# Optimization experiments

Hardware: AMD Instinct MI355X
Metric: run time of the kernel (lower is better)

## Reference

```python
import jax, jax.numpy as jnp
import numpy as np

E = 256

def setup_inputs() -> dict:
    key = jax.random.key(0)
    ks = jax.random.split(key, 10)
    N, T_y, T_x = 8, 300, 160
    s = 1.0 / np.sqrt(E)  # torch-style uniform-ish init scale, keeps gates unsaturated
    return {
        "inputs": jax.random.normal(ks[0], (N, T_y, E // 2), jnp.float32),
        "memory": jax.random.normal(ks[1], (N, T_x, E), jnp.float32),
        "h0": jnp.zeros((1, N, E), jnp.float32),
        "Wih": jax.random.normal(ks[2], (3 * E, E // 2), jnp.float32) * s,
        "Whh": jax.random.normal(ks[3], (3 * E, E), jnp.float32) * s,
        "bih": jax.random.normal(ks[4], (3 * E,), jnp.float32) * s,
        "bhh": jax.random.normal(ks[5], (3 * E,), jnp.float32) * s,
        "W": jax.random.normal(ks[6], (E, E), jnp.float32) * s,
        "U": jax.random.normal(ks[7], (E, E), jnp.float32) * s,
        "v": jax.random.normal(ks[8], (E,), jnp.float32) * s,
    }


def reference(inputs, memory, h0, Wih, Whh, bih, bhh, W, U, v):
    # GRU (PyTorch gate order r, z, n), batch_first, single layer, unidirectional.
    def step(h, x_t):
        gi = x_t @ Wih.T + bih      # [N, 3E]
        gh = h @ Whh.T + bhh        # [N, 3E]
        ir, iz, i_n = jnp.split(gi, 3, axis=-1)
        hr, hz, hn = jnp.split(gh, 3, axis=-1)
        r = jax.nn.sigmoid(ir + hr)
        z = jax.nn.sigmoid(iz + hz)
        n = jnp.tanh(i_n + r * hn)
        h_new = (1.0 - z) * n + z * h
        return h_new, h_new

    h_last, outs = jax.lax.scan(step, h0[0], jnp.swapaxes(inputs, 0, 1))
    outputs = jnp.swapaxes(outs, 0, 1)   # [N, T_y, E]
    hidden = h_last[None]                # [1, N, E]

    # Bahdanau additive attention
    w = outputs @ W.T                    # [N, T_y, E]
    u = memory @ U.T                     # [N, T_x, E]
    # scores: v . tanh(w + u) broadcast over [N, T_y, T_x, E]
    scores = jnp.einsum('ntxe,e->ntx', jnp.tanh(w[:, :, None, :] + u[:, None, :, :]), v)
    attn_weights = jax.nn.softmax(scores, axis=2)  # [N, T_y, T_x]
    return attn_weights, outputs, hidden
```

## Files before the change

### kernel.cpp

```cpp
#include <hip/hip_runtime.h>


typedef _Float16 f16x2 __attribute__((ext_vector_type(2)));
typedef _Float16 f16x8 __attribute__((ext_vector_type(8)));
typedef float f32x4 __attribute__((ext_vector_type(4)));

__device__ __forceinline__ float fexp2(float x) { return __builtin_amdgcn_exp2f(x); }
__device__ __forceinline__ float frcp(float x) { return __builtin_amdgcn_rcpf(x); }
__device__ __forceinline__ float fsig(float x) {
    return frcp(1.0f + fexp2(x * -1.4426950408889634f));
}
__device__ __forceinline__ float ftanh(float x) {
    return 1.0f - 2.0f * frcp(1.0f + fexp2(x * 2.8853900817779268f));
}

__device__ __forceinline__ float pick4(f32x4 v, int s) {
    float ab = (s & 1) ? v[1] : v[0];
    float cd = (s & 1) ? v[3] : v[2];
    return (s & 2) ? cd : ab;
}

__global__ __launch_bounds__(256) void phase1_kernel(
    const float* __restrict__ Whh, unsigned* __restrict__ wd,
    const float* __restrict__ inputs, const float* __restrict__ Wih,
    float* __restrict__ gi, const float* __restrict__ bih,
    const float* __restrict__ bhh, int* flags, int full) {
    if (full && blockIdx.x == 0 && threadIdx.x < 10) flags[threadIdx.x] = 0;
    if (blockIdx.x < 384) {
        int gid = blockIdx.x * 256 + threadIdx.x;
        int i = gid >> 9, t = gid & 511;
        int fi = i >> 2, j = i & 3;
        int g = fi >> 4, m2 = (fi >> 3) & 1, ks = fi & 7;
        int w = t >> 6, l = t & 63;
        int row = 256 * g + 32 * w + 16 * m2 + (l & 15);
        int k = 32 * ks + 8 * (l >> 4) + 2 * j;
        union { unsigned u; f16x2 h; } cv;
        cv.h[0] = (_Float16)Whh[(size_t)row * 256 + k];
        cv.h[1] = (_Float16)Whh[(size_t)row * 256 + k + 1];
        wd[i * 512 + t] = cv.u;
        return;
    }
    int id = blockIdx.x - 384;
    const int n0 = (id % 12) * 64, m0 = (id / 12) * 64;
    __shared__ float Xs[32][65];
    __shared__ float Ws2[32][65];
    const int tid = threadIdx.x;
    const int tx = tid & 15, ty = tid >> 4;
    const int M = 2400, K = 128;
    float acc[4][4] = {};
    for (int k0 = 0; k0 < K; k0 += 32) {
#pragma unroll
        for (int i = 0; i < 8; ++i) {
            int e = tid + i * 256;
            int kk = e & 31, m = e >> 5;
            int row = m0 + m;
            Xs[kk][m] = (row < M) ? inputs[(size_t)row * K + k0 + kk] : 0.0f;
            Ws2[kk][m] = Wih[(size_t)(n0 + m) * K + k0 + kk];
        }
        __syncthreads();
#pragma unroll
        for (int kk = 0; kk < 32; ++kk) {
            float a[4], b[4];
#pragma unroll
            for (int i = 0; i < 4; ++i) a[i] = Xs[kk][ty * 4 + i];
#pragma unroll
            for (int j = 0; j < 4; ++j) b[j] = Ws2[kk][tx * 4 + j];
#pragma unroll
            for (int i = 0; i < 4; ++i)
#pragma unroll
                for (int j = 0; j < 4; ++j) acc[i][j] += a[i] * b[j];
        }
        __syncthreads();
    }
#pragma unroll
    for (int i = 0; i < 4; ++i) {
        int row = m0 + ty * 4 + i;
        if (row >= M) continue;
        int b = row / 300;
        int t = row - b * 300;
#pragma unroll
        for (int j = 0; j < 4; ++j) {
            int col = n0 + tx * 4 + j;
            float val = acc[i][j] + ((col < 512) ? (bih[col] + bhh[col]) : bih[col]);
            gi[(size_t)(t * 8 + b) * 768 + col] = val;
        }
    }
}

__global__ __launch_bounds__(256) void gemm_kernel(
    const float* __restrict__ X, const float* __restrict__ Wt,
    float* __restrict__ C, _Float16* __restrict__ C16,
    int M, int N, int K, int mode) {
    __shared__ float Xs[32][65];
    __shared__ float Ws2[32][65];
    const int n0 = blockIdx.x * 64, m0 = blockIdx.y * 64;
    const int tid = threadIdx.x;
    const int tx = tid & 15, ty = tid >> 4;
    float acc[4][4] = {};
    for (int k0 = 0; k0 < K; k0 += 32) {
#pragma unroll
        for (int i = 0; i < 8; ++i) {
            int e = tid + i * 256;
            int kk = e & 31, m = e >> 5;
            int row = m0 + m;
            Xs[kk][m] = (row < M) ? X[(size_t)row * K + k0 + kk] : 0.0f;
            Ws2[kk][m] = Wt[(size_t)(n0 + m) * K + k0 + kk];
        }
        __syncthreads();
#pragma unroll
        for (int kk = 0; kk < 32; ++kk) {
            float a[4], b[4];
#pragma unroll
            for (int i = 0; i < 4; ++i) a[i] = Xs[kk][ty * 4 + i];
#pragma unroll
            for (int j = 0; j < 4; ++j) b[j] = Ws2[kk][tx * 4 + j];
#pragma unroll
            for (int i = 0; i < 4; ++i)
#pragma unroll
                for (int j = 0; j < 4; ++j) acc[i][j] += a[i] * b[j];
        }
        __syncthreads();
    }
#pragma unroll
    for (int i = 0; i < 4; ++i) {
        int row = m0 + ty * 4 + i;
        if (row >= M) continue;
#pragma unroll
        for (int j = 0; j < 4; ++j) {
            int col = n0 + tx * 4 + j;
            if (mode == 2) C16[(size_t)row * N + col] = (_Float16)acc[i][j];
            else           C[(size_t)row * N + col] = acc[i][j];
        }
    }
}

__global__ __launch_bounds__(512, 1) void gru_mega(
    const float* __restrict__ gi, const unsigned* __restrict__ wd,
    const float* __restrict__ h0, const float* __restrict__ bhh,
    float* __restrict__ outs, float* __restrict__ hid,
    const float* __restrict__ memory, const float* __restrict__ Um,
    _Float16* __restrict__ u16, const float* __restrict__ W,
    const float* __restrict__ vv, float* __restrict__ attn,
    int* flags, int full) {
    __shared__ __align__(16) _Float16 hbuf[2][256];
    __shared__ float Xs[32][65];
    __shared__ float Ws2[32][65];
    __shared__ unsigned uS[160 * 129];
    __shared__ __align__(16) float oL[10][260];
    __shared__ float wLf[10][256];
    __shared__ float vL[256], sc[160], red[2];

    const int tid = threadIdx.x;

    if (blockIdx.x >= 8) {
        int id = blockIdx.x - 8;
        if (id < 80) {
            const int n0 = (id & 3) * 64, m0 = (id >> 2) * 64;
            const int tx = tid & 15, ty = (tid & 255) >> 4;
            float acc[4][4] = {};
            for (int k0 = 0; k0 < 256; k0 += 32) {
                if (tid < 256) {
#pragma unroll
                    for (int i = 0; i < 8; ++i) {
                        int e = tid + i * 256;
                        int kk = e & 31, m = e >> 5;
                        Xs[kk][m] = memory[(size_t)(m0 + m) * 256 + k0 + kk];
                        Ws2[kk][m] = Um[(size_t)(n0 + m) * 256 + k0 + kk];
                    }
                }
                __syncthreads();
                if (tid < 256) {
#pragma unroll
                    for (int kk = 0; kk < 32; ++kk) {
                        float a[4], b[4];
#pragma unroll
                        for (int i = 0; i < 4; ++i) a[i] = Xs[kk][ty * 4 + i];
#pragma unroll
                        for (int j = 0; j < 4; ++j) b[j] = Ws2[kk][tx * 4 + j];
#pragma unroll
                        for (int i = 0; i < 4; ++i)
#pragma unroll
                            for (int j = 0; j < 4; ++j) acc[i][j] += a[i] * b[j];
                    }
                }
                __syncthreads();
            }
            if (tid < 256) {
#pragma unroll
                for (int i = 0; i < 4; ++i)
#pragma unroll
                    for (int j = 0; j < 4; ++j)
                        u16[(size_t)(m0 + ty * 4 + i) * 256 + n0 + tx * 4 + j] =
                            (_Float16)acc[i][j];
            }
            if (!full) return;
            __syncthreads();
            if (tid == 0)
                __hip_atomic_fetch_add(&flags[8], 1, __ATOMIC_RELEASE,
                                       __HIP_MEMORY_SCOPE_AGENT);
        }
        if (!full) return;

        const int grp = id / 30;
        const int tc = id % 30;
        if (tid == 0) {
            while (__hip_atomic_load(&flags[8], __ATOMIC_RELAXED,
                                     __HIP_MEMORY_SCOPE_AGENT) < 80)
                __builtin_amdgcn_s_sleep(32);
            while (__hip_atomic_load(&flags[8], __ATOMIC_ACQUIRE,
                                     __HIP_MEMORY_SCOPE_AGENT) < 80)
                __builtin_amdgcn_s_sleep(8);
        }
        __syncthreads();
        const unsigned* ug = (const unsigned*)(u16 + (size_t)grp * 160 * 256);
        for (int i = tid; i < 20480; i += 512)
            uS[(i >> 7) * 129 + (i & 127)] = ug[i];
        if (tid < 256) vL[tid] = vv[tid];
        __syncthreads();

        if (tid == 0) {
            while (__hip_atomic_load(&flags[grp], __ATOMIC_RELAXED,
                                     __HIP_MEMORY_SCOPE_AGENT) < 1)
                __builtin_amdgcn_s_sleep(32);
            while (__hip_atomic_load(&flags[grp], __ATOMIC_ACQUIRE,
                                     __HIP_MEMORY_SCOPE_AGENT) < 1)
                __builtin_amdgcn_s_sleep(8);
        }
        __syncthreads();
        for (int i = tid; i < 2560; i += 512) {
            int ti = i >> 8, k = i & 255;
            oL[ti][k] = outs[((size_t)grp * 300 + tc * 10 + ti) * 256 + k];
        }
        __syncthreads();
        if (tid < 256) {
            float a0 = 0, a1 = 0, a2 = 0, a3 = 0, a4 = 0;
            float a5 = 0, a6 = 0, a7 = 0, a8 = 0, a9 = 0;
            for (int k4 = 0; k4 < 256; k4 += 4) {
                float4 wq = *(const float4*)(W + (size_t)tid * 256 + k4);
#define WROW(ACC, TI)                                                     \
                {                                                         \
                    float4 oq = *(const float4*)(&oL[TI][k4]);            \
                    ACC += wq.x * oq.x + wq.y * oq.y +                    \
                           wq.z * oq.z + wq.w * oq.w;                     \
                }
                WROW(a0, 0) WROW(a1, 1) WROW(a2, 2) WROW(a3, 3) WROW(a4, 4)
                WROW(a5, 5) WROW(a6, 6) WROW(a7, 7) WROW(a8, 8) WROW(a9, 9)
#undef WROW
            }
            wLf[0][tid] = a0; wLf[1][tid] = a1; wLf[2][tid] = a2;
            wLf[3][tid] = a3; wLf[4][tid] = a4; wLf[5][tid] = a5;
            wLf[6][tid] = a6; wLf[7][tid] = a7; wLf[8][tid] = a8;
            wLf[9][tid] = a9;
        }
        __syncthreads();
        for (int ti = 0; ti < 10; ++ti) {
            int t = tc * 10 + ti;
            float acc2 = 0.0f;
            if (tid < 160) {
                const unsigned* ur = uS + tid * 129;
                const float* wl = wLf[ti];
#pragma unroll 8
                for (int e2 = 0; e2 < 128; ++e2) {
                    union { unsigned uu2; _Float16 hh[2]; } cv;
                    cv.uu2 = ur[e2];
                    int ee = e2 * 2;
                    acc2 += vL[ee] * ftanh(wl[ee] + (float)cv.hh[0]);
                    acc2 += vL[ee + 1] * ftanh(wl[ee + 1] + (float)cv.hh[1]);
                }
                sc[tid] = acc2;
            }
            __syncthreads();
            if (tid < 64) {
                float m = -3.0e38f;
                for (int i = tid; i < 160; i += 64) m = fmaxf(m, sc[i]);
#pragma unroll
                for (int o = 32; o; o >>= 1) m = fmaxf(m, __shfl_xor(m, o));
                if (tid == 0) red[0] = m;
            }
            __syncthreads();
            float ee = 0.0f;
            if (tid < 160) {
                ee = fexp2((acc2 - red[0]) * 1.4426950408889634f);
                sc[tid] = ee;
            }
            __syncthreads();
            if (tid < 64) {
                float s = 0.0f;
                for (int i = tid; i < 160; i += 64) s += sc[i];
#pragma unroll
                for (int o = 32; o; o >>= 1) s += __shfl_xor(s, o);
                if (tid == 0) red[1] = s;
            }
            __syncthreads();
            if (tid < 160)
                attn[(size_t)(grp * 300 + t) * 160 + tid] = ee * frcp(red[1]);
            __syncthreads();
        }
        return;
    }

    const int b = blockIdx.x;
    const int t = tid;
    const int w = t >> 6, l = t & 63;
    const int grp = l >> 4;
    const int sel = l & 7;
    const int hi = (l >> 3) & 1;
    const int m2s = sel >> 2, rsel = sel & 3;
    const int e = 32 * w + 16 * m2s + 4 * grp + rsel;

    f16x8 wf[48];
#pragma unroll
    for (int fi = 0; fi < 48; ++fi) {
        union { unsigned u[4]; f16x8 v; } cv;
#pragma unroll
        for (int j = 0; j < 4; ++j) cv.u[j] = wd[(fi * 4 + j) * 512 + t];
        wf[fi] = cv.v;
    }

    float h = h0[b * 256 + e];
    float bn = bhh[512 + e];
    if (!hi) hbuf[0][e] = (_Float16)h;
    const float* gp = gi + b * 768;
    float* op = outs + (size_t)b * 76800 + e;

    float gr = gp[e], gz = gp[e + 256], gn = gp[e + 512];
    __syncthreads();

    for (int st = 0; st < 300; ++st) {
        int stn = (st < 299) ? st + 1 : st;
        const float* g = gp + (size_t)stn * 6144;
        float grn = g[e], gzn = g[e + 256], gnn = g[e + 512];

        const _Float16* hb = hbuf[st & 1];
        f16x8 hv0 = *(const f16x8*)(hb + 0 * 32 + 8 * grp);
        f16x8 hv1 = *(const f16x8*)(hb + 1 * 32 + 8 * grp);
        f16x8 hv2 = *(const f16x8*)(hb + 2 * 32 + 8 * grp);
        f16x8 hv3 = *(const f16x8*)(hb + 3 * 32 + 8 * grp);
        f16x8 hv4 = *(const f16x8*)(hb + 4 * 32 + 8 * grp);
        f16x8 hv5 = *(const f16x8*)(hb + 5 * 32 + 8 * grp);
        f16x8 hv6 = *(const f16x8*)(hb + 6 * 32 + 8 * grp);
        f16x8 hv7 = *(const f16x8*)(hb + 7 * 32 + 8 * grp);

        f32x4 aR0 = {0.f, 0.f, 0.f, 0.f}, aR1 = {0.f, 0.f, 0.f, 0.f};
        f32x4 aZ0 = {0.f, 0.f, 0.f, 0.f}, aZ1 = {0.f, 0.f, 0.f, 0.f};
        f32x4 aN0 = {0.f, 0.f, 0.f, 0.f}, aN1 = {0.f, 0.f, 0.f, 0.f};
#define KSTEP(ks, hv)                                                        \
        aR0 = __builtin_amdgcn_mfma_f32_16x16x32_f16(wf[0 * 8 + ks], hv, aR0, 0, 0, 0); \
        aR1 = __builtin_amdgcn_mfma_f32_16x16x32_f16(wf[1 * 8 + ks], hv, aR1, 0, 0, 0); \
        aZ0 = __builtin_amdgcn_mfma_f32_16x16x32_f16(wf[2 * 8 + ks], hv, aZ0, 0, 0, 0); \
        aZ1 = __builtin_amdgcn_mfma_f32_16x16x32_f16(wf[3 * 8 + ks], hv, aZ1, 0, 0, 0); \
        aN0 = __builtin_amdgcn_mfma_f32_16x16x32_f16(wf[4 * 8 + ks], hv, aN0, 0, 0, 0); \
        aN1 = __builtin_amdgcn_mfma_f32_16x16x32_f16(wf[5 * 8 + ks], hv, aN1, 0, 0, 0);
        KSTEP(0, hv0) KSTEP(1, hv1) KSTEP(2, hv2) KSTEP(3, hv3)
        KSTEP(4, hv4) KSTEP(5, hv5) KSTEP(6, hv6) KSTEP(7, hv7)
#undef KSTEP

        f32x4 vR = m2s ? aR1 : aR0;
        f32x4 vZ = m2s ? aZ1 : aZ0;
        f32x4 vN = m2s ? aN1 : aN0;
        float sr = pick4(vR, rsel);
        float sz = pick4(vZ, rsel);
        float sn = pick4(vN, rsel);

        float r = fsig(gr + sr);
        float z = fsig(gz + sz);
        float n = ftanh(gn + r * (sn + bn));
        h = n + z * (h - n);

        gr = grn; gz = gzn; gn = gnn;

        if (hi)
            op[st * 256] = h;
        else
            hbuf[(st + 1) & 1][e] = (_Float16)h;
        asm volatile("s_waitcnt lgkmcnt(0)\n\ts_barrier" ::: "memory");
    }
    if (!hi) hid[b * 256 + e] = h;
    if (full) {
        asm volatile("s_waitcnt vmcnt(0)" ::: "memory");
        __syncthreads();
        if (t == 0)
            __hip_atomic_store(&flags[b], 1, __ATOMIC_RELEASE,
                               __HIP_MEMORY_SCOPE_AGENT);
    }
}

__global__ __launch_bounds__(256) void attn_kernel(
    const _Float16* __restrict__ u16, const float* __restrict__ wv,
    const float* __restrict__ v, float* __restrict__ attn) {
    const int tc = blockIdx.x, b = blockIdx.y;
    const int tid = threadIdx.x;
    __shared__ float wL[256], vL[256], sc[160], red[2];
    __shared__ unsigned uS[160 * 129];

    const unsigned* ug = (const unsigned*)(u16 + (size_t)b * 160 * 256);
    for (int i = tid; i < 20480; i += 256)
        uS[(i >> 7) * 129 + (i & 127)] = ug[i];
    vL[tid] = v[tid];

    for (int ti = 0; ti < 10; ++ti) {
        int t = tc * 10 + ti;
        wL[tid] = wv[(size_t)(b * 300 + t) * 256 + tid];
        __syncthreads();
        float acc = 0.0f;
        if (tid < 160) {
            const unsigned* ur = uS + tid * 129;
#pragma unroll 8
            for (int e2 = 0; e2 < 128; ++e2) {
                union { unsigned uu; _Float16 hh[2]; } cv;
                cv.uu = ur[e2];
                int ee = e2 * 2;
                acc += vL[ee] * ftanh(wL[ee] + (float)cv.hh[0]);
                acc += vL[ee + 1] * ftanh(wL[ee + 1] + (float)cv.hh[1]);
            }
            sc[tid] = acc;
        }
        __syncthreads();
        if (tid < 64) {
            float m = -3.0e38f;
            for (int i = tid; i < 160; i += 64) m = fmaxf(m, sc[i]);
#pragma unroll
            for (int o = 32; o; o >>= 1) m = fmaxf(m, __shfl_xor(m, o));
            if (tid == 0) red[0] = m;
        }
        __syncthreads();
        float ee = 0.0f;
        if (tid < 160) {
            ee = fexp2((acc - red[0]) * 1.4426950408889634f);
            sc[tid] = ee;
        }
        __syncthreads();
        if (tid < 64) {
            float s = 0.0f;
            for (int i = tid; i < 160; i += 64) s += sc[i];
#pragma unroll
            for (int o = 32; o; o >>= 1) s += __shfl_xor(s, o);
            if (tid == 0) red[1] = s;
        }
        __syncthreads();
        if (tid < 160)
            attn[(size_t)(b * 300 + t) * 160 + tid] = ee * frcp(red[1]);
        __syncthreads();
    }
}

extern "C" void kernel_launch(void* const* d_in, const int* in_sizes, int n_in,
                              void* d_out, int out_size, void* d_ws, size_t ws_size,
                              hipStream_t stream) {
    const float* inputs = (const float*)d_in[0];
    const float* memory = (const float*)d_in[1];
    const float* h0 = (const float*)d_in[2];
    const float* Wih = (const float*)d_in[3];
    const float* Whh = (const float*)d_in[4];
    const float* bih = (const float*)d_in[5];
    const float* bhh = (const float*)d_in[6];
    const float* Wm = (const float*)d_in[7];
    const float* Um = (const float*)d_in[8];
    const float* vv = (const float*)d_in[9];

    float* out = (float*)d_out;
    float* out_attn = out;
    float* out_outputs = out + 384000;
    float* out_hidden = out + 998400;

    char* ws = (char*)d_ws;
    float* gi = (float*)ws;
    unsigned* wd = (unsigned*)(ws + 7372800);

    const size_t U16_OFF = 7766016, FLAG_OFF = 8421376;
    const bool full = ws_size >= FLAG_OFF + 64;
    _Float16* u16 = full ? (_Float16*)(ws + U16_OFF) : (_Float16*)ws;
    int* flags = (int*)(ws + FLAG_OFF);

    phase1_kernel<<<840, 256, 0, stream>>>(Whh, wd, inputs, Wih, gi, bih, bhh,
                                           flags, full ? 1 : 0);
    if (full) {
        gru_mega<<<248, 512, 0, stream>>>(gi, wd, h0, bhh, out_outputs,
                                          out_hidden, memory, Um, u16, Wm, vv,
                                          out_attn, flags, 1);
    } else {
        float* wbuf = (float*)(ws + 655360);
        gru_mega<<<8, 512, 0, stream>>>(gi, wd, h0, bhh, out_outputs,
                                        out_hidden, memory, Um, u16, Wm, vv,
                                        out_attn, flags, 0);
        gemm_kernel<<<dim3(4, 20), 256, 0, stream>>>(memory, Um, nullptr, u16,
                                                     1280, 256, 256, 2);
        gemm_kernel<<<dim3(4, 38), 256, 0, stream>>>(out_outputs, Wm, wbuf,
                                                     nullptr, 2400, 256, 256, 0);
        attn_kernel<<<dim3(30, 8), 256, 0, stream>>>(u16, wbuf, vv, out_attn);
    }
}
```

Measured before the change: 467.6 us.

## Split attention work across all 512 threads and pad sync flags to cache lines

In the fused attention consumer blocks, the W projection now uses all 512 threads, each half computing five of the ten rows. The score loop splits the embedding dimension across 320 threads, with partial sums combined through shared memory at the cost of an extra barrier. Sync flags are spaced 32 ints apart to avoid false sharing, and spin sleep intervals are lengthened. The fallback path fuses the W GEMM into a new wattn kernel, which changes the required workspace size.

```diff
diff --git a/kernel.cpp b/kernel.cpp
--- a/kernel.cpp
+++ b/kernel.cpp
@@ -19,13 +19,16 @@
     float cd = (s & 1) ? v[3] : v[2];
     return (s & 2) ? cd : ab;
 }
+
+#define FLAG(i) ((i) * 32)
 
 __global__ __launch_bounds__(256) void phase1_kernel(
     const float* __restrict__ Whh, unsigned* __restrict__ wd,
     const float* __restrict__ inputs, const float* __restrict__ Wih,
     float* __restrict__ gi, const float* __restrict__ bih,
     const float* __restrict__ bhh, int* flags, int full) {
-    if (full && blockIdx.x == 0 && threadIdx.x < 10) flags[threadIdx.x] = 0;
+    if (full && blockIdx.x == 0 && threadIdx.x < 9)
+        flags[FLAG(threadIdx.x)] = 0;
     if (blockIdx.x < 384) {
         int gid = blockIdx.x * 256 + threadIdx.x;
         int i = gid >> 9, t = gid & 511;
@@ -148,7 +151,7 @@
     __shared__ unsigned uS[160 * 129];
     __shared__ __align__(16) float oL[10][260];
     __shared__ float wLf[10][256];
-    __shared__ float vL[256], sc[160], red[2];
+    __shared__ float vL[256], scP[2][160], sc[160], red[2];
 
     const int tid = threadIdx.x;
 
@@ -196,7 +199,7 @@
             if (!full) return;
             __syncthreads();
             if (tid == 0)
-                __hip_atomic_fetch_add(&flags[8], 1, __ATOMIC_RELEASE,
+                __hip_atomic_fetch_add(&flags[FLAG(8)], 1, __ATOMIC_RELEASE,
                                        __HIP_MEMORY_SCOPE_AGENT);
         }
         if (!full) return;
@@ -204,10 +207,10 @@
         const int grp = id / 30;
         const int tc = id % 30;
         if (tid == 0) {
-            while (__hip_atomic_load(&flags[8], __ATOMIC_RELAXED,
+            while (__hip_atomic_load(&flags[FLAG(8)], __ATOMIC_RELAXED,
                                      __HIP_MEMORY_SCOPE_AGENT) < 80)
-                __builtin_amdgcn_s_sleep(32);
-            while (__hip_atomic_load(&flags[8], __ATOMIC_ACQUIRE,
+                __builtin_amdgcn_s_sleep(64);
+            while (__hip_atomic_load(&flags[FLAG(8)], __ATOMIC_ACQUIRE,
                                      __HIP_MEMORY_SCOPE_AGENT) < 80)
                 __builtin_amdgcn_s_sleep(8);
         }
@@ -219,10 +222,10 @@
         __syncthreads();
 
         if (tid == 0) {
-            while (__hip_atomic_load(&flags[grp], __ATOMIC_RELAXED,
+            while (__hip_atomic_load(&flags[FLAG(grp)], __ATOMIC_RELAXED,
                                      __HIP_MEMORY_SCOPE_AGENT) < 1)
-                __builtin_amdgcn_s_sleep(32);
-            while (__hip_atomic_load(&flags[grp], __ATOMIC_ACQUIRE,
+                __builtin_amdgcn_s_sleep(127);
+            while (__hip_atomic_load(&flags[FLAG(grp)], __ATOMIC_ACQUIRE,
                                      __HIP_MEMORY_SCOPE_AGENT) < 1)
                 __builtin_amdgcn_s_sleep(8);
         }
@@ -232,43 +235,47 @@
             oL[ti][k] = outs[((size_t)grp * 300 + tc * 10 + ti) * 256 + k];
         }
         __syncthreads();
-        if (tid < 256) {
+        {
+            const int c = tid & 255, rh = tid >> 8;
             float a0 = 0, a1 = 0, a2 = 0, a3 = 0, a4 = 0;
-            float a5 = 0, a6 = 0, a7 = 0, a8 = 0, a9 = 0;
+            const float* wr = W + (size_t)c * 256;
+            const int r0 = rh * 5;
             for (int k4 = 0; k4 < 256; k4 += 4) {
-                float4 wq = *(const float4*)(W + (size_t)tid * 256 + k4);
+                float4 wq = *(const float4*)(wr + k4);
 #define WROW(ACC, TI)                                                     \
                 {                                                         \
                     float4 oq = *(const float4*)(&oL[TI][k4]);            \
                     ACC += wq.x * oq.x + wq.y * oq.y +                    \
                            wq.z * oq.z + wq.w * oq.w;                     \
                 }
-                WROW(a0, 0) WROW(a1, 1) WROW(a2, 2) WROW(a3, 3) WROW(a4, 4)
-                WROW(a5, 5) WROW(a6, 6) WROW(a7, 7) WROW(a8, 8) WROW(a9, 9)
+                WROW(a0, r0 + 0) WROW(a1, r0 + 1) WROW(a2, r0 + 2)
+                WROW(a3, r0 + 3) WROW(a4, r0 + 4)
 #undef WROW
             }
-            wLf[0][tid] = a0; wLf[1][tid] = a1; wLf[2][tid] = a2;
-            wLf[3][tid] = a3; wLf[4][tid] = a4; wLf[5][tid] = a5;
-            wLf[6][tid] = a6; wLf[7][tid] = a7; wLf[8][tid] = a8;
-            wLf[9][tid] = a9;
+            wLf[r0 + 0][c] = a0; wLf[r0 + 1][c] = a1; wLf[r0 + 2][c] = a2;
+            wLf[r0 + 3][c] = a3; wLf[r0 + 4][c] = a4;
         }
         __syncthreads();
         for (int ti = 0; ti < 10; ++ti) {
-            int t = tc * 10 + ti;
-            float acc2 = 0.0f;
-            if (tid < 160) {
-                const unsigned* ur = uS + tid * 129;
-                const float* wl = wLf[ti];
+            if (tid < 320) {
+                const int x = (tid < 160) ? tid : tid - 160;
+                const int half = (tid >= 160) ? 1 : 0;
+                const unsigned* ur = uS + x * 129 + half * 64;
+                const float* wl = wLf[ti] + half * 128;
+                const float* vl = vL + half * 128;
+                float acc2 = 0.0f;
 #pragma unroll 8
-                for (int e2 = 0; e2 < 128; ++e2) {
+                for (int e2 = 0; e2 < 64; ++e2) {
                     union { unsigned uu2; _Float16 hh[2]; } cv;
                     cv.uu2 = ur[e2];
                     int ee = e2 * 2;
-                    acc2 += vL[ee] * ftanh(wl[ee] + (float)cv.hh[0]);
-                    acc2 += vL[ee + 1] * ftanh(wl[ee + 1] + (float)cv.hh[1]);
+                    acc2 += vl[ee] * ftanh(wl[ee] + (float)cv.hh[0]);
+                    acc2 += vl[ee + 1] * ftanh(wl[ee + 1] + (float)cv.hh[1]);
                 }
-                sc[tid] = acc2;
-            }
+                scP[half][x] = acc2;
+            }
+            __syncthreads();
+            if (tid < 160) sc[tid] = scP[0][tid] + scP[1][tid];
             __syncthreads();
             if (tid < 64) {
                 float m = -3.0e38f;
@@ -280,7 +287,7 @@
             __syncthreads();
             float ee = 0.0f;
             if (tid < 160) {
-                ee = fexp2((acc2 - red[0]) * 1.4426950408889634f);
+                ee = fexp2((sc[tid] - red[0]) * 1.4426950408889634f);
                 sc[tid] = ee;
             }
             __syncthreads();
@@ -293,7 +300,8 @@
             }
             __syncthreads();
             if (tid < 160)
-                attn[(size_t)(grp * 300 + t) * 160 + tid] = ee * frcp(red[1]);
+                attn[(size_t)(grp * 300 + tc * 10 + ti) * 160 + tid] =
+                    ee * frcp(red[1]);
             __syncthreads();
         }
         return;
@@ -380,40 +388,67 @@
         asm volatile("s_waitcnt vmcnt(0)" ::: "memory");
         __syncthreads();
         if (t == 0)
-            __hip_atomic_store(&flags[b], 1, __ATOMIC_RELEASE,
+            __hip_atomic_store(&flags[FLAG(b)], 1, __ATOMIC_RELEASE,
                                __HIP_MEMORY_SCOPE_AGENT);
     }
 }
 
-__global__ __launch_bounds__(256) void attn_kernel(
-    const _Float16* __restrict__ u16, const float* __restrict__ wv,
-    const float* __restrict__ v, float* __restrict__ attn) {
+__global__ __launch_bounds__(256) void wattn_kernel(
+    const _Float16* __restrict__ u16, const float* __restrict__ outs,
+    const float* __restrict__ W, const float* __restrict__ vv,
+    float* __restrict__ attn) {
     const int tc = blockIdx.x, b = blockIdx.y;
     const int tid = threadIdx.x;
-    __shared__ float wL[256], vL[256], sc[160], red[2];
     __shared__ unsigned uS[160 * 129];
+    __shared__ __align__(16) float oL[10][260];
+    __shared__ float wLf[10][256];
+    __shared__ float vL[256], sc[160], red[2];
 
     const unsigned* ug = (const unsigned*)(u16 + (size_t)b * 160 * 256);
     for (int i = tid; i < 20480; i += 256)
         uS[(i >> 7) * 129 + (i & 127)] = ug[i];
-    vL[tid] = v[tid];
-
+    vL[tid] = vv[tid];
+    for (int i = tid; i < 2560; i += 256) {
+        int ti = i >> 8, k = i & 255;
+        oL[ti][k] = outs[((size_t)b * 300 + tc * 10 + ti) * 256 + k];
+    }
+    __syncthreads();
+    {
+        float a0 = 0, a1 = 0, a2 = 0, a3 = 0, a4 = 0;
+        float a5 = 0, a6 = 0, a7 = 0, a8 = 0, a9 = 0;
+        for (int k4 = 0; k4 < 256; k4 += 4) {
+            float4 wq = *(const float4*)(W + (size_t)tid * 256 + k4);
+#define WROW(ACC, TI)                                                     \
+            {                                                             \
+                float4 oq = *(const float4*)(&oL[TI][k4]);                \
+                ACC += wq.x * oq.x + wq.y * oq.y +                        \
+                       wq.z * oq.z + wq.w * oq.w;                        \
+            }
+            WROW(a0, 0) WROW(a1, 1) WROW(a2, 2) WROW(a3, 3) WROW(a4, 4)
+            WROW(a5, 5) WROW(a6, 6) WROW(a7, 7) WROW(a8, 8) WROW(a9, 9)
+#undef WROW
+        }
+        wLf[0][tid] = a0; wLf[1][tid] = a1; wLf[2][tid] = a2;
+        wLf[3][tid] = a3; wLf[4][tid] = a4; wLf[5][tid] = a5;
+        wLf[6][tid] = a6; wLf[7][tid] = a7; wLf[8][tid] = a8;
+        wLf[9][tid] = a9;
+    }
+    __syncthreads();
     for (int ti = 0; ti < 10; ++ti) {
         int t = tc * 10 + ti;
-        wL[tid] = wv[(size_t)(b * 300 + t) * 256 + tid];
-        __syncthreads();
-        float acc = 0.0f;
+        float acc2 = 0.0f;
         if (tid < 160) {
             const unsigned* ur = uS + tid * 129;
+            const float* wl = wLf[ti];
 #pragma unroll 8
             for (int e2 = 0; e2 < 128; ++e2) {
-                union { unsigned uu; _Float16 hh[2]; } cv;
-                cv.uu = ur[e2];
+                union { unsigned uu2; _Float16 hh[2]; } cv;
+                cv.uu2 = ur[e2];
                 int ee = e2 * 2;
-                acc += vL[ee] * ftanh(wL[ee] + (float)cv.hh[0]);
-                acc += vL[ee + 1] * ftanh(wL[ee + 1] + (float)cv.hh[1]);
-            }
-            sc[tid] = acc;
+                acc2 += vL[ee] * ftanh(wl[ee] + (float)cv.hh[0]);
+                acc2 += vL[ee + 1] * ftanh(wl[ee + 1] + (float)cv.hh[1]);
+            }
+            sc[tid] = acc2;
         }
         __syncthreads();
         if (tid < 64) {
@@ -426,7 +461,7 @@
         __syncthreads();
         float ee = 0.0f;
         if (tid < 160) {
-            ee = fexp2((acc - red[0]) * 1.4426950408889634f);
+            ee = fexp2((acc2 - red[0]) * 1.4426950408889634f);
             sc[tid] = ee;
         }
         __syncthreads();
@@ -468,7 +503,7 @@
     unsigned* wd = (unsigned*)(ws + 7372800);
 
     const size_t U16_OFF = 7766016, FLAG_OFF = 8421376;
-    const bool full = ws_size >= FLAG_OFF + 64;
+    const bool full = ws_size >= FLAG_OFF + 1152;
     _Float16* u16 = full ? (_Float16*)(ws + U16_OFF) : (_Float16*)ws;
     int* flags = (int*)(ws + FLAG_OFF);
 
@@ -479,14 +514,12 @@
                                           out_hidden, memory, Um, u16, Wm, vv,
                                           out_attn, flags, 1);
     } else {
-        float* wbuf = (float*)(ws + 655360);
         gru_mega<<<8, 512, 0, stream>>>(gi, wd, h0, bhh, out_outputs,
                                         out_hidden, memory, Um, u16, Wm, vv,
                                         out_attn, flags, 0);
         gemm_kernel<<<dim3(4, 20), 256, 0, stream>>>(memory, Um, nullptr, u16,
                                                      1280, 256, 256, 2);
-        gemm_kernel<<<dim3(4, 38), 256, 0, stream>>>(out_outputs, Wm, wbuf,
-                                                     nullptr, 2400, 256, 256, 0);
-        attn_kernel<<<dim3(30, 8), 256, 0, stream>>>(u16, wbuf, vv, out_attn);
-    }
-}
+        wattn_kernel<<<dim3(30, 8), 256, 0, stream>>>(u16, out_outputs, Wm, vv,
+                                                      out_attn);
+    }
+}
```

New measurement: 464.3 us. Within noise of the previous version (-0.7%).
